# Kernel optimization log

Hardware: AMD Instinct MI355X
Metric: run time of the kernel (lower is better)

Reference implementation:

```python
import jax, jax.numpy as jnp
import numpy as np

HEADS = 12
FEATURES = 768
D_HEAD = FEATURES // HEADS
SCALE = float(np.sqrt(D_HEAD))
EPS = 1e-12
N = 2048


def setup_inputs() -> dict:
    key = jax.random.key(0)
    ks = jax.random.split(key, 5)
    init = 1.0 / np.sqrt(FEATURES)
    return {
        "x": jax.random.normal(ks[0], (N, FEATURES), dtype=jnp.float32),
        "Wq": jax.random.normal(ks[1], (FEATURES, FEATURES), dtype=jnp.float32) * init,
        "Wk": jax.random.normal(ks[2], (FEATURES, FEATURES), dtype=jnp.float32) * init,
        "Wv": jax.random.normal(ks[3], (FEATURES, FEATURES), dtype=jnp.float32) * init,
        "Wo": jax.random.normal(ks[4], (FEATURES, FEATURES), dtype=jnp.float32) * init,
        "gamma": jnp.ones((FEATURES,), dtype=jnp.float32),
        "beta": jnp.zeros((FEATURES,), dtype=jnp.float32),
    }


def reference(x, Wq, Wk, Wv, Wo, gamma, beta):
    n = x.shape[0]
    # projections (no bias); weight layout [out, in] -> x @ W.T
    q = (x @ Wq.T).reshape(n, HEADS, D_HEAD).transpose(1, 0, 2)  # [h, n, d]
    k = (x @ Wk.T).reshape(n, HEADS, D_HEAD).transpose(1, 0, 2)
    v = (x @ Wv.T).reshape(n, HEADS, D_HEAD).transpose(1, 0, 2)
    # scores [h, n, n]; original divides q@k^T by sqrt(d_head)
    att = jnp.einsum("hnd,hmd->hnm", q, k) / SCALE
    att = jax.nn.softmax(att, axis=-1)  # dropout p=0 -> identity
    out = jnp.einsum("hnm,hmd->hnd", att, v)  # [h, n, d]
    out = out.transpose(1, 0, 2).reshape(n, FEATURES)  # n (h d)
    out = out @ Wo.T
    # residual + layernorm (eps=1e-12)
    y = out + x
    mu = jnp.mean(y, axis=-1, keepdims=True)
    var = jnp.mean((y - mu) ** 2, axis=-1, keepdims=True)
    return (y - mu) / jnp.sqrt(var + EPS) * gamma + beta
```

## Files before the change

kernel.cpp:

```cpp
#include <hip/hip_runtime.h>
#include <hip/hip_bf16.h>
#include <math.h>

#define N_TOK 2048
#define FEAT  768
#define HEADS 12
#define DHEAD 64
#define SPLIT 4
#define KV_PER (N_TOK / SPLIT)

typedef __bf16 v8bf __attribute__((ext_vector_type(8)));
typedef __bf16 v4bf __attribute__((ext_vector_type(4)));
typedef float  v4f  __attribute__((ext_vector_type(4)));

#define XE ((size_t)N_TOK * FEAT)
#define WE ((size_t)FEAT * FEAT)
#define QK_LD 1536

#define SCALE_FOLD 0.18033688011112042f

__device__ __forceinline__ void gload16(const __bf16* g, __bf16* l) {
    __builtin_amdgcn_global_load_lds(
        (const __attribute__((address_space(1))) unsigned int*)g,
        (__attribute__((address_space(3))) unsigned int*)l, 16, 0, 0);
}

__global__ __launch_bounds__(256) void cvt_all(
        const float* __restrict__ x,  const float* __restrict__ Wq,
        const float* __restrict__ Wk, const float* __restrict__ Wv,
        const float* __restrict__ Wo,
        __bf16* __restrict__ xb, __bf16* __restrict__ wqkv, __bf16* __restrict__ wob) {
    size_t i = ((size_t)blockIdx.x * 256 + threadIdx.x) * 4;
    const float* src; __bf16* dst; size_t off; float scale = 1.f;
    if (i < XE)               { src = x;  dst = xb;          off = i; }
    else if (i < XE + WE)     { src = Wq; dst = wqkv;        off = i - XE; scale = SCALE_FOLD; }
    else if (i < XE + 2 * WE) { src = Wk; dst = wqkv + WE;   off = i - XE - WE; }
    else if (i < XE + 3 * WE) { src = Wv; dst = wqkv + 2*WE; off = i - XE - 2*WE; }
    else                      { src = Wo; dst = wob;         off = i - XE - 3*WE; }
    float4 v = *(const float4*)(src + off);
    v4bf o;
    o[0] = (__bf16)(v.x * scale); o[1] = (__bf16)(v.y * scale);
    o[2] = (__bf16)(v.z * scale); o[3] = (__bf16)(v.w * scale);
    *(v4bf*)(dst + off) = o;
}

__global__ __launch_bounds__(256) void gemm_qkv(
        const __bf16* __restrict__ A, const __bf16* __restrict__ B,
        __bf16* __restrict__ qk, __bf16* __restrict__ vt) {
    __shared__ __bf16 As[128][32];
    __shared__ __bf16 Bs[128][32];
    const int t    = threadIdx.x;
    const int lane = t & 63, w = t >> 6;
    const int quad = lane >> 4, l15 = lane & 15;
    const int wm = w & 1, wn = w >> 1;
    const int bm = blockIdx.y * 128, bn = blockIdx.x * 128;
    const int srow = lane >> 2, scol = (lane & 3) * 8;

    v4f acc[4][4] = {};
    for (int k0 = 0; k0 < FEAT; k0 += 32) {
        gload16(A + (size_t)(bm + w * 32 + srow) * FEAT + k0 + scol,      &As[w * 32][0]);
        gload16(A + (size_t)(bm + w * 32 + 16 + srow) * FEAT + k0 + scol, &As[w * 32 + 16][0]);
        gload16(B + (size_t)(bn + w * 32 + srow) * FEAT + k0 + scol,      &Bs[w * 32][0]);
        gload16(B + (size_t)(bn + w * 32 + 16 + srow) * FEAT + k0 + scol, &Bs[w * 32 + 16][0]);
        __syncthreads();
        v8bf a[4], b[4];
#pragma unroll
        for (int mi = 0; mi < 4; mi++) a[mi] = *(const v8bf*)&As[wm * 64 + mi * 16 + l15][quad * 8];
#pragma unroll
        for (int ni = 0; ni < 4; ni++) b[ni] = *(const v8bf*)&Bs[wn * 64 + ni * 16 + l15][quad * 8];
#pragma unroll
        for (int mi = 0; mi < 4; mi++)
#pragma unroll
            for (int ni = 0; ni < 4; ni++)
                acc[mi][ni] = __builtin_amdgcn_mfma_f32_16x16x32_bf16(a[mi], b[ni], acc[mi][ni], 0, 0, 0);
        __syncthreads();
    }
    if (bn < 2 * FEAT) {
#pragma unroll
        for (int mi = 0; mi < 4; mi++)
#pragma unroll
            for (int ni = 0; ni < 4; ni++) {
                int col = bn + wn * 64 + ni * 16 + l15;
#pragma unroll
                for (int r = 0; r < 4; r++) {
                    int row = bm + wm * 64 + mi * 16 + quad * 4 + r;
                    qk[(size_t)row * QK_LD + col] = (__bf16)acc[mi][ni][r];
                }
            }
    } else {
#pragma unroll
        for (int mi = 0; mi < 4; mi++)
#pragma unroll
            for (int ni = 0; ni < 4; ni++) {
                int col = bn + wn * 64 + ni * 16 + l15 - 2 * FEAT;
                int row = bm + wm * 64 + mi * 16 + quad * 4;
                v4bf pk;
#pragma unroll
                for (int r = 0; r < 4; r++) pk[r] = (__bf16)acc[mi][ni][r];
                *(v4bf*)(vt + (size_t)col * N_TOK + row) = pk;
            }
    }
}

__global__ __launch_bounds__(256, 3) void attention(
        const __bf16* __restrict__ QK, const __bf16* __restrict__ vt,
        __bf16* __restrict__ Opart, float* __restrict__ lpart) {
    __shared__ __bf16 KV[2][2][64][64];
    __shared__ __bf16 PT[4][32][64];
    const int t    = threadIdx.x;
    const int lane = t & 63, w = t >> 6;
    const int quad = lane >> 4, l15 = lane & 15;
    const int h = blockIdx.y, s = blockIdx.z;
    const int q0 = blockIdx.x * 128 + w * 32;
    const int sw = (l15 & 7) * 8;

    v8bf qf[2][2];
#pragma unroll
    for (int qt = 0; qt < 2; qt++) {
        const __bf16* qp = QK + (size_t)(q0 + qt * 16 + l15) * QK_LD + h * DHEAD + quad * 8;
        qf[qt][0] = *(const v8bf*)qp;
        qf[qt][1] = *(const v8bf*)(qp + 32);
    }
    const __bf16* kg = QK + FEAT + h * DHEAD;
    const __bf16* vg = vt + (size_t)(h * DHEAD) * N_TOK;

    v4f o_acc[4][2] = {};
    float lacc[2] = {0.f, 0.f};

    const int kvbeg = s * KV_PER;
    const int lr8 = lane >> 3;

    auto stage = [&](int b, int kv0) {
#pragma unroll
        for (int i = 0; i < 2; i++) {
            int row = w * 16 + i * 8 + lr8;
            int gs  = (lane & 7) ^ (row & 7);
            gload16(kg + (size_t)(kv0 + row) * QK_LD + gs * 8, &KV[b][0][w * 16 + i * 8][0]);
            gload16(vg + (size_t)row * N_TOK + kv0 + gs * 8,   &KV[b][1][w * 16 + i * 8][0]);
        }
    };

    auto step = [&](int b) {
        v8bf kf[4][2];
#pragma unroll
        for (int kvt = 0; kvt < 4; kvt++)
#pragma unroll
            for (int ks = 0; ks < 2; ks++)
                kf[kvt][ks] = *(const v8bf*)&KV[b][0][kvt * 16 + l15][((ks * 4 + quad) ^ (l15 & 7)) * 8];
        v4f sv[4][2];
#pragma unroll
        for (int kvt = 0; kvt < 4; kvt++)
#pragma unroll
            for (int qt = 0; qt < 2; qt++) {
                v4f a = {};
                a = __builtin_amdgcn_mfma_f32_16x16x32_bf16(kf[kvt][0], qf[qt][0], a, 0, 0, 0);
                a = __builtin_amdgcn_mfma_f32_16x16x32_bf16(kf[kvt][1], qf[qt][1], a, 0, 0, 0);
                sv[kvt][qt] = a;
            }
#pragma unroll
        for (int kvt = 0; kvt < 4; kvt++)
#pragma unroll
            for (int qt = 0; qt < 2; qt++) {
                float p0 = __builtin_amdgcn_exp2f(sv[kvt][qt][0]);
                float p1 = __builtin_amdgcn_exp2f(sv[kvt][qt][1]);
                float p2 = __builtin_amdgcn_exp2f(sv[kvt][qt][2]);
                float p3 = __builtin_amdgcn_exp2f(sv[kvt][qt][3]);
                lacc[qt] += (p0 + p1) + (p2 + p3);
                v4bf pk;
                pk[0] = (__bf16)p0; pk[1] = (__bf16)p1; pk[2] = (__bf16)p2; pk[3] = (__bf16)p3;
                *(v4bf*)&PT[w][qt * 16 + l15][(kvt * 16 + quad * 4) ^ sw] = pk;
            }
        v8bf vf[2][4];
#pragma unroll
        for (int ks = 0; ks < 2; ks++)
#pragma unroll
            for (int dt = 0; dt < 4; dt++)
                vf[ks][dt] = *(const v8bf*)&KV[b][1][dt * 16 + l15][((ks * 4 + quad) ^ (l15 & 7)) * 8];
        v8bf ptf[2][2];
#pragma unroll
        for (int ks = 0; ks < 2; ks++)
#pragma unroll
            for (int qt = 0; qt < 2; qt++)
                ptf[ks][qt] = *(const v8bf*)&PT[w][qt * 16 + l15][(ks * 32 + quad * 8) ^ sw];
#pragma unroll
        for (int dt = 0; dt < 4; dt++)
#pragma unroll
            for (int ks = 0; ks < 2; ks++)
#pragma unroll
                for (int qt = 0; qt < 2; qt++)
                    o_acc[dt][qt] = __builtin_amdgcn_mfma_f32_16x16x32_bf16(vf[ks][dt], ptf[ks][qt], o_acc[dt][qt], 0, 0, 0);
    };

    stage(0, kvbeg);
    const int TILES = KV_PER / 64;
    for (int tt = 0; tt < TILES; tt++) {
        __syncthreads();
        if (tt + 1 < TILES) stage((tt + 1) & 1, kvbeg + (tt + 1) * 64);
        step(tt & 1);
    }

    __bf16* op = Opart + (size_t)s * XE;
#pragma unroll
    for (int qt = 0; qt < 2; qt++) {
        float l = lacc[qt];
        l += __shfl_xor(l, 16); l += __shfl_xor(l, 32);
        float linv = 1.0f / l;
        int q = q0 + qt * 16 + l15;
        if (quad == 0) lpart[((size_t)s * HEADS + h) * N_TOK + q] = l;
#pragma unroll
        for (int dt = 0; dt < 4; dt++) {
            v4bf pk;
#pragma unroll
            for (int r = 0; r < 4; r++) pk[r] = (__bf16)(o_acc[dt][qt][r] * linv);
            *(v4bf*)(op + (size_t)q * FEAT + h * DHEAD + dt * 16 + quad * 4) = pk;
        }
    }
}

__global__ __launch_bounds__(256) void gemm_out(
        const __bf16* __restrict__ Op, const float* __restrict__ lp,
        const __bf16* __restrict__ Wo, const float* __restrict__ x,
        float* __restrict__ Yf) {
    __shared__ __bf16 As[64][32];
    __shared__ __bf16 Bs[128][32];
    const int t    = threadIdx.x;
    const int lane = t & 63, w = t >> 6;
    const int quad = lane >> 4, l15 = lane & 15;
    const int wm = w & 1, wn = w >> 1;
    const int bm = blockIdx.y * 64, bn = blockIdx.x * 128;
    const int srow = lane >> 2, scol = (lane & 3) * 8;

    const int ar = t >> 2, ac = (t & 3) * 8;
    const int arow = bm + ar;

    v4f acc[2][4] = {};
    for (int k0 = 0; k0 < FEAT; k0 += 32) {
        {
            int h = (k0 + ac) >> 6;
            float ls[SPLIT], tot = 0.f;
#pragma unroll
            for (int s = 0; s < SPLIT; s++) {
                ls[s] = lp[((size_t)s * HEADS + h) * N_TOK + arow];
                tot += ls[s];
            }
            float inv = 1.0f / tot;
            float a8[8] = {};
#pragma unroll
            for (int s = 0; s < SPLIT; s++) {
                v8bf p = *(const v8bf*)(Op + (size_t)s * XE + (size_t)arow * FEAT + k0 + ac);
                float wgt = ls[s] * inv;
#pragma unroll
                for (int j = 0; j < 8; j++) a8[j] += wgt * (float)p[j];
            }
            v8bf av;
#pragma unroll
            for (int j = 0; j < 8; j++) av[j] = (__bf16)a8[j];
            *(v8bf*)&As[ar][ac] = av;
        }
        gload16(Wo + (size_t)(bn + w * 32 + srow) * FEAT + k0 + scol,      &Bs[w * 32][0]);
        gload16(Wo + (size_t)(bn + w * 32 + 16 + srow) * FEAT + k0 + scol, &Bs[w * 32 + 16][0]);
        __syncthreads();
        v8bf a[2], b[4];
#pragma unroll
        for (int mi = 0; mi < 2; mi++) a[mi] = *(const v8bf*)&As[wm * 32 + mi * 16 + l15][quad * 8];
#pragma unroll
        for (int ni = 0; ni < 4; ni++) b[ni] = *(const v8bf*)&Bs[wn * 64 + ni * 16 + l15][quad * 8];
#pragma unroll
        for (int mi = 0; mi < 2; mi++)
#pragma unroll
            for (int ni = 0; ni < 4; ni++)
                acc[mi][ni] = __builtin_amdgcn_mfma_f32_16x16x32_bf16(a[mi], b[ni], acc[mi][ni], 0, 0, 0);
        __syncthreads();
    }
#pragma unroll
    for (int mi = 0; mi < 2; mi++)
#pragma unroll
        for (int ni = 0; ni < 4; ni++) {
            int col = bn + wn * 64 + ni * 16 + l15;
#pragma unroll
            for (int r = 0; r < 4; r++) {
                int row = bm + wm * 32 + mi * 16 + quad * 4 + r;
                Yf[(size_t)row * FEAT + col] = acc[mi][ni][r] + x[(size_t)row * FEAT + col];
            }
        }
}

__global__ __launch_bounds__(256) void ln_kernel(
        const float* __restrict__ Y, const float* __restrict__ gamma,
        const float* __restrict__ beta, float* __restrict__ out) {
    __shared__ float sbuf[4];
    const int row = blockIdx.x, t = threadIdx.x;
    const float* y = Y + (size_t)row * FEAT;
    float v0 = y[t], v1 = y[t + 256], v2 = y[t + 512];
    float s = v0 + v1 + v2;
#pragma unroll
    for (int m = 32; m; m >>= 1) s += __shfl_xor(s, m);
    if ((t & 63) == 0) sbuf[t >> 6] = s;
    __syncthreads();
    float mean = (sbuf[0] + sbuf[1] + sbuf[2] + sbuf[3]) * (1.f / FEAT);
    __syncthreads();
    float d0 = v0 - mean, d1 = v1 - mean, d2 = v2 - mean;
    float q = d0 * d0 + d1 * d1 + d2 * d2;
#pragma unroll
    for (int m = 32; m; m >>= 1) q += __shfl_xor(q, m);
    if ((t & 63) == 0) sbuf[t >> 6] = q;
    __syncthreads();
    float var = (sbuf[0] + sbuf[1] + sbuf[2] + sbuf[3]) * (1.f / FEAT);
    float rs = rsqrtf(var + 1e-12f);
    float* o = out + (size_t)row * FEAT;
    o[t]       = d0 * rs * gamma[t]       + beta[t];
    o[t + 256] = d1 * rs * gamma[t + 256] + beta[t + 256];
    o[t + 512] = d2 * rs * gamma[t + 512] + beta[t + 512];
}

extern "C" void kernel_launch(void* const* d_in, const int* in_sizes, int n_in,
                              void* d_out, int out_size, void* d_ws, size_t ws_size,
                              hipStream_t stream) {
    const float* x     = (const float*)d_in[0];
    const float* Wq    = (const float*)d_in[1];
    const float* Wk    = (const float*)d_in[2];
    const float* Wv    = (const float*)d_in[3];
    const float* Wo    = (const float*)d_in[4];
    const float* gamma = (const float*)d_in[5];
    const float* beta  = (const float*)d_in[6];
    float* out = (float*)d_out;

    char* ws = (char*)d_ws;
    size_t off = 0;
    auto alloc = [&](size_t bytes) -> void* {
        void* p = ws + off;
        off += (bytes + 255) & ~(size_t)255;
        return p;
    };
    __bf16* xb   = (__bf16*)alloc(XE * 2);
    __bf16* wqkv = (__bf16*)alloc(3 * WE * 2);
    __bf16* wob  = (__bf16*)alloc(WE * 2);
    __bf16* qk   = (__bf16*)alloc((size_t)N_TOK * QK_LD * 2);
    __bf16* vtb  = (__bf16*)alloc((size_t)FEAT * N_TOK * 2);
    __bf16* Op   = (__bf16*)alloc(SPLIT * XE * 2);
    float*  lp   = (float*)alloc(SPLIT * HEADS * N_TOK * 4);
    float*  Yf   = (float*)ws;

    cvt_all<<<(int)((XE + 4 * WE) / 4 / 256), 256, 0, stream>>>(x, Wq, Wk, Wv, Wo, xb, wqkv, wob);

    gemm_qkv<<<dim3((QK_LD + FEAT) / 128, N_TOK / 128), 256, 0, stream>>>(xb, wqkv, qk, vtb);

    attention<<<dim3(N_TOK / 128, HEADS, SPLIT), 256, 0, stream>>>(qk, vtb, Op, lp);

    gemm_out<<<dim3(FEAT / 128, N_TOK / 64), 256, 0, stream>>>(Op, lp, wob, x, Yf);

    ln_kernel<<<N_TOK, 256, 0, stream>>>(Yf, gamma, beta, out);
}
```

Before: 151.2 us.

## Merge split-KV attention partials with float atomics and shrink QKV GEMM M-tile

Each attention split now atomically adds its unnormalized output and row sums into one fp32 accumulator, which is zeroed with a memset beforehand. This replaces the per-split bf16 partial buffers and the weighted reduction that gemm_out used to do, so gemm_out reads one fp32 tile and divides by the summed l. Separately, the QKV GEMM tile shrinks from 128 to 64 rows, doubling the block count for better CU occupancy. The price is many scattered global float atomics, an extra memset, and nondeterministic summation order.

```diff
diff --git a/kernel.cpp b/kernel.cpp
--- a/kernel.cpp
+++ b/kernel.cpp
@@ -47,29 +47,28 @@
 __global__ __launch_bounds__(256) void gemm_qkv(
         const __bf16* __restrict__ A, const __bf16* __restrict__ B,
         __bf16* __restrict__ qk, __bf16* __restrict__ vt) {
-    __shared__ __bf16 As[128][32];
+    __shared__ __bf16 As[64][32];
     __shared__ __bf16 Bs[128][32];
     const int t    = threadIdx.x;
     const int lane = t & 63, w = t >> 6;
     const int quad = lane >> 4, l15 = lane & 15;
     const int wm = w & 1, wn = w >> 1;
-    const int bm = blockIdx.y * 128, bn = blockIdx.x * 128;
+    const int bm = blockIdx.y * 64, bn = blockIdx.x * 128;
     const int srow = lane >> 2, scol = (lane & 3) * 8;
 
-    v4f acc[4][4] = {};
+    v4f acc[2][4] = {};
     for (int k0 = 0; k0 < FEAT; k0 += 32) {
-        gload16(A + (size_t)(bm + w * 32 + srow) * FEAT + k0 + scol,      &As[w * 32][0]);
-        gload16(A + (size_t)(bm + w * 32 + 16 + srow) * FEAT + k0 + scol, &As[w * 32 + 16][0]);
+        gload16(A + (size_t)(bm + w * 16 + srow) * FEAT + k0 + scol,      &As[w * 16][0]);
         gload16(B + (size_t)(bn + w * 32 + srow) * FEAT + k0 + scol,      &Bs[w * 32][0]);
         gload16(B + (size_t)(bn + w * 32 + 16 + srow) * FEAT + k0 + scol, &Bs[w * 32 + 16][0]);
         __syncthreads();
-        v8bf a[4], b[4];
-#pragma unroll
-        for (int mi = 0; mi < 4; mi++) a[mi] = *(const v8bf*)&As[wm * 64 + mi * 16 + l15][quad * 8];
+        v8bf a[2], b[4];
+#pragma unroll
+        for (int mi = 0; mi < 2; mi++) a[mi] = *(const v8bf*)&As[wm * 32 + mi * 16 + l15][quad * 8];
 #pragma unroll
         for (int ni = 0; ni < 4; ni++) b[ni] = *(const v8bf*)&Bs[wn * 64 + ni * 16 + l15][quad * 8];
 #pragma unroll
-        for (int mi = 0; mi < 4; mi++)
+        for (int mi = 0; mi < 2; mi++)
 #pragma unroll
             for (int ni = 0; ni < 4; ni++)
                 acc[mi][ni] = __builtin_amdgcn_mfma_f32_16x16x32_bf16(a[mi], b[ni], acc[mi][ni], 0, 0, 0);
@@ -77,23 +76,23 @@
     }
     if (bn < 2 * FEAT) {
 #pragma unroll
-        for (int mi = 0; mi < 4; mi++)
+        for (int mi = 0; mi < 2; mi++)
 #pragma unroll
             for (int ni = 0; ni < 4; ni++) {
                 int col = bn + wn * 64 + ni * 16 + l15;
 #pragma unroll
                 for (int r = 0; r < 4; r++) {
-                    int row = bm + wm * 64 + mi * 16 + quad * 4 + r;
+                    int row = bm + wm * 32 + mi * 16 + quad * 4 + r;
                     qk[(size_t)row * QK_LD + col] = (__bf16)acc[mi][ni][r];
                 }
             }
     } else {
 #pragma unroll
-        for (int mi = 0; mi < 4; mi++)
+        for (int mi = 0; mi < 2; mi++)
 #pragma unroll
             for (int ni = 0; ni < 4; ni++) {
                 int col = bn + wn * 64 + ni * 16 + l15 - 2 * FEAT;
-                int row = bm + wm * 64 + mi * 16 + quad * 4;
+                int row = bm + wm * 32 + mi * 16 + quad * 4;
                 v4bf pk;
 #pragma unroll
                 for (int r = 0; r < 4; r++) pk[r] = (__bf16)acc[mi][ni][r];
@@ -104,7 +103,7 @@
 
 __global__ __launch_bounds__(256, 3) void attention(
         const __bf16* __restrict__ QK, const __bf16* __restrict__ vt,
-        __bf16* __restrict__ Opart, float* __restrict__ lpart) {
+        float* __restrict__ Osum, float* __restrict__ Lsum) {
     __shared__ __bf16 KV[2][2][64][64];
     __shared__ __bf16 PT[4][32][64];
     const int t    = threadIdx.x;
@@ -199,27 +198,22 @@
         step(tt & 1);
     }
 
-    __bf16* op = Opart + (size_t)s * XE;
 #pragma unroll
     for (int qt = 0; qt < 2; qt++) {
-        float l = lacc[qt];
-        l += __shfl_xor(l, 16); l += __shfl_xor(l, 32);
-        float linv = 1.0f / l;
         int q = q0 + qt * 16 + l15;
-        if (quad == 0) lpart[((size_t)s * HEADS + h) * N_TOK + q] = l;
-#pragma unroll
-        for (int dt = 0; dt < 4; dt++) {
-            v4bf pk;
-#pragma unroll
-            for (int r = 0; r < 4; r++) pk[r] = (__bf16)(o_acc[dt][qt][r] * linv);
-            *(v4bf*)(op + (size_t)q * FEAT + h * DHEAD + dt * 16 + quad * 4) = pk;
-        }
+        unsafeAtomicAdd(&Lsum[(size_t)h * N_TOK + q], lacc[qt]);
+        float* op = Osum + (size_t)q * FEAT + h * DHEAD + quad * 4;
+#pragma unroll
+        for (int dt = 0; dt < 4; dt++)
+#pragma unroll
+            for (int r = 0; r < 4; r++)
+                unsafeAtomicAdd(op + dt * 16 + r, o_acc[dt][qt][r]);
     }
 }
 
 __global__ __launch_bounds__(256) void gemm_out(
-        const __bf16* __restrict__ Op, const float* __restrict__ lp,
-        const __bf16* __restrict__ Wo, const float* __restrict__ x,
+        const float* __restrict__ Osum, const float* __restrict__ Lsum,
+        const __bf16* __restrict__ Wo,  const float* __restrict__ x,
         float* __restrict__ Yf) {
     __shared__ __bf16 As[64][32];
     __shared__ __bf16 Bs[128][32];
@@ -237,24 +231,14 @@
     for (int k0 = 0; k0 < FEAT; k0 += 32) {
         {
             int h = (k0 + ac) >> 6;
-            float ls[SPLIT], tot = 0.f;
-#pragma unroll
-            for (int s = 0; s < SPLIT; s++) {
-                ls[s] = lp[((size_t)s * HEADS + h) * N_TOK + arow];
-                tot += ls[s];
-            }
-            float inv = 1.0f / tot;
-            float a8[8] = {};
-#pragma unroll
-            for (int s = 0; s < SPLIT; s++) {
-                v8bf p = *(const v8bf*)(Op + (size_t)s * XE + (size_t)arow * FEAT + k0 + ac);
-                float wgt = ls[s] * inv;
-#pragma unroll
-                for (int j = 0; j < 8; j++) a8[j] += wgt * (float)p[j];
-            }
+            float inv = 1.0f / Lsum[(size_t)h * N_TOK + arow];
+            const float* apf = Osum + (size_t)arow * FEAT + k0 + ac;
+            float4 a0 = *(const float4*)apf, a1 = *(const float4*)(apf + 4);
             v8bf av;
-#pragma unroll
-            for (int j = 0; j < 8; j++) av[j] = (__bf16)a8[j];
+            av[0] = (__bf16)(a0.x * inv); av[1] = (__bf16)(a0.y * inv);
+            av[2] = (__bf16)(a0.z * inv); av[3] = (__bf16)(a0.w * inv);
+            av[4] = (__bf16)(a1.x * inv); av[5] = (__bf16)(a1.y * inv);
+            av[6] = (__bf16)(a1.z * inv); av[7] = (__bf16)(a1.w * inv);
             *(v8bf*)&As[ar][ac] = av;
         }
         gload16(Wo + (size_t)(bn + w * 32 + srow) * FEAT + k0 + scol,      &Bs[w * 32][0]);
@@ -337,17 +321,19 @@
     __bf16* wob  = (__bf16*)alloc(WE * 2);
     __bf16* qk   = (__bf16*)alloc((size_t)N_TOK * QK_LD * 2);
     __bf16* vtb  = (__bf16*)alloc((size_t)FEAT * N_TOK * 2);
-    __bf16* Op   = (__bf16*)alloc(SPLIT * XE * 2);
-    float*  lp   = (float*)alloc(SPLIT * HEADS * N_TOK * 4);
+    float*  Osum = (float*)alloc((XE + HEADS * N_TOK) * 4);
+    float*  Lsum = Osum + XE;
     float*  Yf   = (float*)ws;
 
+    hipMemsetAsync(Osum, 0, (XE + HEADS * N_TOK) * 4, stream);
+
     cvt_all<<<(int)((XE + 4 * WE) / 4 / 256), 256, 0, stream>>>(x, Wq, Wk, Wv, Wo, xb, wqkv, wob);
 
-    gemm_qkv<<<dim3((QK_LD + FEAT) / 128, N_TOK / 128), 256, 0, stream>>>(xb, wqkv, qk, vtb);
-
-    attention<<<dim3(N_TOK / 128, HEADS, SPLIT), 256, 0, stream>>>(qk, vtb, Op, lp);
-
-    gemm_out<<<dim3(FEAT / 128, N_TOK / 64), 256, 0, stream>>>(Op, lp, wob, x, Yf);
+    gemm_qkv<<<dim3((QK_LD + FEAT) / 128, N_TOK / 64), 256, 0, stream>>>(xb, wqkv, qk, vtb);
+
+    attention<<<dim3(N_TOK / 128, HEADS, SPLIT), 256, 0, stream>>>(qk, vtb, Osum, Lsum);
+
+    gemm_out<<<dim3(FEAT / 128, N_TOK / 64), 256, 0, stream>>>(Osum, Lsum, wob, x, Yf);
 
     ln_kernel<<<N_TOK, 256, 0, stream>>>(Yf, gamma, beta, out);
 }
```

New measurement: 216.2 us. 1.43x slower.
